# Kernel tuning notes

Hardware: AMD Instinct MI355X
Metric: run time of the kernel (lower is better)

Reference implementation:

```python
import jax, jax.numpy as jnp
import numpy as np

B, T, H = 2, 1024, 4096
HK, HV, DK, DV = 8, 32, 64, 64
VPK = HV // HK            # value heads per key head = 4
KEY_DIM = HK * DK         # 512
VAL_DIM = HV * DV         # 2048
CONV_DIM = 2 * KEY_DIM + VAL_DIM  # 3072
KSZ = 4
EPS = 1e-5
L2_EPS = 1e-6


def _l2norm(x):
    return x * jax.lax.rsqrt(jnp.sum(x * x, axis=-1, keepdims=True) + L2_EPS)


def setup_inputs() -> dict:
    key = jax.random.key(0)
    ks = jax.random.split(key, 8)
    s = 0.02
    return {
        "hidden_states": jax.random.normal(ks[0], (B, T, H), jnp.float32),
        "W_qkvz": jax.random.normal(ks[1], (H, 2 * KEY_DIM + 2 * VAL_DIM), jnp.float32) * s,
        "W_ba": jax.random.normal(ks[2], (H, 2 * HV), jnp.float32) * s,
        "conv_w": jax.random.normal(ks[3], (CONV_DIM, KSZ), jnp.float32) * 0.1,
        "dt_bias": jnp.ones((HV,), jnp.float32),
        "A_log": jnp.log(jax.random.uniform(ks[4], (HV,), jnp.float32, 1.0, 16.0)),
        "norm_w": jnp.ones((DV,), jnp.float32),
        "W_out": jax.random.normal(ks[5], (VAL_DIM, H), jnp.float32) * s,
    }


def _forward(hidden_states, W_qkvz, W_ba, conv_w, dt_bias, A_log, norm_w, W_out):
    # --- projections ---
    qkvz = hidden_states @ W_qkvz                       # [B,T,5120]
    ba = hidden_states @ W_ba                           # [B,T,64]
    # fix_query_key_value_ordering: per key head [q(Dk), k(Dk), v(vpk*Dv), z(vpk*Dv)]
    qkvz = qkvz.reshape(B, T, HK, 2 * DK + 2 * VPK * DV)
    q = qkvz[..., :DK]                                  # [B,T,HK,DK]
    k = qkvz[..., DK:2 * DK]
    v = qkvz[..., 2 * DK:2 * DK + VPK * DV].reshape(B, T, HV, DV)
    z = qkvz[..., 2 * DK + VPK * DV:].reshape(B, T, HV, DV)
    ba = ba.reshape(B, T, HK, 2 * VPK)
    b = ba[..., :VPK].reshape(B, T, HV)
    a = ba[..., VPK:].reshape(B, T, HV)

    # --- causal depthwise conv over concatenated qkv, then silu ---
    mixed = jnp.concatenate(
        [q.reshape(B, T, KEY_DIM), k.reshape(B, T, KEY_DIM), v.reshape(B, T, VAL_DIM)], axis=-1)
    padded = jnp.pad(mixed, ((0, 0), (KSZ - 1, 0), (0, 0)))
    conv = sum(padded[:, j:j + T, :] * conv_w[:, j] for j in range(KSZ))
    conv = jax.nn.silu(conv)
    q = conv[..., :KEY_DIM].reshape(B, T, HK, DK)
    k = conv[..., KEY_DIM:2 * KEY_DIM].reshape(B, T, HK, DK)
    v = conv[..., 2 * KEY_DIM:].reshape(B, T, HV, DV)

    # --- fused GDN gating: g = -exp(A_log)*softplus(a+dt_bias), beta = sigmoid(b) ---
    g = -jnp.exp(A_log) * jax.nn.softplus(a + dt_bias)  # [B,T,HV]
    beta = jax.nn.sigmoid(b)                            # [B,T,HV]

    # --- q/k l2 norm + scale, broadcast key heads to value heads ---
    q = _l2norm(q) * (DK ** -0.5)
    k = _l2norm(k)
    q = jnp.repeat(q, VPK, axis=2)                      # [B,T,HV,DK]
    k = jnp.repeat(k, VPK, axis=2)

    # --- gated delta-rule recurrence over time ---
    def step(S, inp):
        qt, kt, vt, gt, bt = inp                        # qt/kt [B,HV,DK], vt [B,HV,DV]
        S = S * jnp.exp(gt)[..., None, None]            # decay
        pred = jnp.einsum('bhk,bhkv->bhv', kt, S)
        delta = (vt - pred) * bt[..., None]
        S = S + jnp.einsum('bhk,bhv->bhkv', kt, delta)
        o = jnp.einsum('bhk,bhkv->bhv', qt, S)
        return S, o

    xs = (q.transpose(1, 0, 2, 3), k.transpose(1, 0, 2, 3), v.transpose(1, 0, 2, 3),
          g.transpose(1, 0, 2), beta.transpose(1, 0, 2))
    S0 = jnp.zeros((B, HV, DK, DV), q.dtype)
    _, o = jax.lax.scan(step, S0, xs)                   # [T,B,HV,DV]
    o = o.transpose(1, 0, 2, 3)                         # [B,T,HV,DV]

    # --- gated RMSNorm (norm before gate) + out projection ---
    o_n = o * jax.lax.rsqrt(jnp.mean(o * o, axis=-1, keepdims=True) + EPS) * norm_w
    o_n = o_n * jax.nn.silu(z)
    return o_n.reshape(B, T, VAL_DIM) @ W_out           # [B,T,H]


def reference(hidden_states, W_qkvz, W_ba, conv_w, dt_bias, A_log, norm_w, W_out):
    return _forward(hidden_states, W_qkvz, W_ba, conv_w, dt_bias, A_log, norm_w, W_out)
```

## Files before the change

kernel.cpp:

```cpp
#include <hip/hip_runtime.h>
#include <hip/hip_bf16.h>
#include <cstdint>
#include <cstddef>


typedef __attribute__((ext_vector_type(8))) short short8;
typedef __attribute__((ext_vector_type(4))) float f32x4;

__device__ __forceinline__ short f2bf(float f) {
  union { float f; unsigned u; } x; x.f = f;
  unsigned r = x.u + 0x7fffu + ((x.u >> 16) & 1u);
  return (short)(r >> 16);
}

__device__ __forceinline__ void gl_lds16(const short* g, short* l) {
  __builtin_amdgcn_global_load_lds(
      (const __attribute__((address_space(1))) void*)g,
      (__attribute__((address_space(3))) void*)l, 16, 0, 0);
}

__global__ __launch_bounds__(256) void to_bf16_kernel(const float* __restrict__ x,
                                                      short* __restrict__ y) {
  int i = blockIdx.x * 256 + threadIdx.x;
  float4 v = ((const float4*)x)[i];
  ushort4 r;
  r.x = (unsigned short)f2bf(v.x);
  r.y = (unsigned short)f2bf(v.y);
  r.z = (unsigned short)f2bf(v.z);
  r.w = (unsigned short)f2bf(v.w);
  ((ushort4*)y)[i] = r;
}

__global__ __launch_bounds__(256) void transpose_w1(const float* __restrict__ Wq,
                                                    const float* __restrict__ Wba,
                                                    short* __restrict__ Wt) {
  __shared__ float tile[32][33];
  int n0 = blockIdx.x * 32;
  int k0 = blockIdx.y * 32;
  int t = threadIdx.x;
  int r = t >> 5;
  int c = t & 31;
#pragma unroll
  for (int i = 0; i < 4; ++i) {
    int kl = r + i * 8;
    int n = n0 + c;
    float v = 0.f;
    if (n < 5120) v = Wq[(size_t)(k0 + kl) * 5120 + n];
    else if (n < 5184) v = Wba[(size_t)(k0 + kl) * 64 + (n - 5120)];
    tile[kl][c] = v;
  }
  __syncthreads();
#pragma unroll
  for (int i = 0; i < 4; ++i) {
    int nl = r + i * 8;
    int kl = c;
    Wt[(size_t)(n0 + nl) * 4096 + k0 + kl] = f2bf(tile[kl][nl]);
  }
}

__global__ __launch_bounds__(256) void transpose_w2(const float* __restrict__ W,
                                                    short* __restrict__ Wt) {
  __shared__ float tile[32][33];
  int n0 = blockIdx.x * 32;
  int k0 = blockIdx.y * 32;
  int t = threadIdx.x;
  int r = t >> 5;
  int c = t & 31;
#pragma unroll
  for (int i = 0; i < 4; ++i) {
    int kl = r + i * 8;
    tile[kl][c] = W[(size_t)(k0 + kl) * 4096 + n0 + c];
  }
  __syncthreads();
#pragma unroll
  for (int i = 0; i < 4; ++i) {
    int nl = r + i * 8;
    int kl = c;
    Wt[(size_t)(n0 + nl) * 2048 + k0 + kl] = f2bf(tile[kl][nl]);
  }
}

template <bool GUARD_N>
__global__ __launch_bounds__(512) void gemm256(const short* __restrict__ A,
                                               const short* __restrict__ Bt,
                                               float* __restrict__ C,
                                               int M, int N, int K) {
  __shared__ __align__(16) short As[3 * 8192];
  __shared__ __align__(16) short Bs[3 * 8192];
  const int tid = threadIdx.x;
  const int w = tid >> 6, lane = tid & 63;
  const int wm = w >> 2, wn = w & 3;
  const int m0 = blockIdx.x * 256, n0 = blockIdx.y * 256;
  (void)M;

  const int p0 = w * 64 + lane;
  const int rp0 = p0 >> 3, q0 = p0 & 7;
  const int mm0 = q0 ^ (rp0 & 7);
  const int srow = rp0 * 2 + (mm0 >> 2);
  const int scol = (mm0 & 3) << 3;
  const short* Ag = A + (size_t)(m0 + srow) * K + scol;
  const short* Bg = Bt + (size_t)(n0 + srow) * K + scol;
  const size_t rstep = (size_t)128 * K;

  const int fr = lane & 15;
  const int s = lane >> 4;
  int aoff[8], boff[4];
#pragma unroll
  for (int i = 0; i < 8; ++i) {
    int row = wm * 128 + i * 16 + fr;
    int rp = row >> 1;
    int q = (((row & 1) << 2) | s) ^ (rp & 7);
    aoff[i] = (rp * 8 + q) * 8;
  }
#pragma unroll
  for (int j = 0; j < 4; ++j) {
    int row = wn * 64 + j * 16 + fr;
    int rp = row >> 1;
    int q = (((row & 1) << 2) | s) ^ (rp & 7);
    boff[j] = (rp * 8 + q) * 8;
  }

  f32x4 acc[8][4];
#pragma unroll
  for (int i = 0; i < 8; ++i)
#pragma unroll
    for (int j = 0; j < 4; ++j) acc[i][j] = (f32x4){0.f, 0.f, 0.f, 0.f};

  const int NKT = K >> 5;

#define STAGE_A(kt, bb)                                                \
  { const short* g = Ag + (size_t)(kt) * 32;                           \
    gl_lds16(g,         &As[(bb) * 8192 + w * 512]);                   \
    gl_lds16(g + rstep, &As[(bb) * 8192 + 4096 + w * 512]); }
#define STAGE_B(kt, bb)                                                \
  { const short* g = Bg + (size_t)(kt) * 32;                           \
    gl_lds16(g,         &Bs[(bb) * 8192 + w * 512]);                   \
    gl_lds16(g + rstep, &Bs[(bb) * 8192 + 4096 + w * 512]); }

  STAGE_A(0, 0); STAGE_B(0, 0);
  STAGE_A(1, 1); STAGE_B(1, 1);
  asm volatile("s_waitcnt vmcnt(4)" ::: "memory");
  __builtin_amdgcn_s_barrier();
  __builtin_amdgcn_sched_barrier(0);

  int bi = 0;
  for (int kt = 0; kt < NKT; ++kt) {
    int bi2 = bi - 1; if (bi2 < 0) bi2 = 2;
    const short* Ab = &As[bi * 8192];
    const short* Bb = &Bs[bi * 8192];
    short8 af[4], bf[4];
#pragma unroll
    for (int i = 0; i < 4; ++i) af[i] = *(const short8*)&Ab[aoff[i]];
#pragma unroll
    for (int j = 0; j < 4; ++j) bf[j] = *(const short8*)&Bb[boff[j]];
    if (kt + 2 < NKT) STAGE_A(kt + 2, bi2);
    __builtin_amdgcn_s_barrier();
    asm volatile("s_waitcnt lgkmcnt(0)" ::: "memory");
    __builtin_amdgcn_sched_barrier(0);
    __builtin_amdgcn_s_setprio(1);
#pragma unroll
    for (int i = 0; i < 4; ++i)
#pragma unroll
      for (int j = 0; j < 4; ++j)
        acc[i][j] = __builtin_amdgcn_mfma_f32_16x16x32_bf16(af[i], bf[j], acc[i][j], 0, 0, 0);
    __builtin_amdgcn_s_setprio(0);
    __builtin_amdgcn_sched_barrier(0);
#pragma unroll
    for (int i = 0; i < 4; ++i) af[i] = *(const short8*)&Ab[aoff[i + 4]];
    if (kt + 2 < NKT) STAGE_B(kt + 2, bi2);
    if (kt < NKT - 2) { asm volatile("s_waitcnt vmcnt(4)" ::: "memory"); }
    else              { asm volatile("s_waitcnt vmcnt(0)" ::: "memory"); }
    __builtin_amdgcn_s_barrier();
    asm volatile("s_waitcnt lgkmcnt(0)" ::: "memory");
    __builtin_amdgcn_sched_barrier(0);
    __builtin_amdgcn_s_setprio(1);
#pragma unroll
    for (int i = 0; i < 4; ++i)
#pragma unroll
      for (int j = 0; j < 4; ++j)
        acc[i + 4][j] = __builtin_amdgcn_mfma_f32_16x16x32_bf16(af[i], bf[j], acc[i + 4][j], 0, 0, 0);
    __builtin_amdgcn_s_setprio(0);
    __builtin_amdgcn_sched_barrier(0);
    __builtin_amdgcn_s_barrier();
    ++bi; if (bi == 3) bi = 0;
  }
#undef STAGE_A
#undef STAGE_B

  const int rbase = (lane >> 4) << 2;
#pragma unroll
  for (int i = 0; i < 8; ++i) {
#pragma unroll
    for (int j = 0; j < 4; ++j) {
      int col = n0 + wn * 64 + j * 16 + fr;
      if (GUARD_N && col >= N) continue;
      int row = m0 + wm * 128 + i * 16 + rbase;
#pragma unroll
      for (int r = 0; r < 4; ++r)
        C[(size_t)(row + r) * N + col] = acc[i][j][r];
    }
  }
}

template <bool GUARD_N>
__global__ __launch_bounds__(256) void gemm128(const short* __restrict__ A,
                                               const short* __restrict__ Bt,
                                               float* __restrict__ C,
                                               int M, int N, int K) {
  __shared__ __align__(16) short As[128 * 32];
  __shared__ __align__(16) short Bs[128 * 32];
  const int tid = threadIdx.x;
  const int wave = tid >> 6;
  const int lane = tid & 63;
  const int m0 = blockIdx.x * 128;
  const int n0 = blockIdx.y * 128;
  const int wm = (wave >> 1) << 6;
  const int wn = (wave & 1) << 6;

  const int srow = (wave << 4) + (lane >> 2);
  const int scol = (lane & 3) << 3;
  const short* Ag = A + (size_t)(m0 + srow) * K + scol;
  const short* Bg = Bt + (size_t)(n0 + srow) * K + scol;
  const size_t rstep = (size_t)64 * K;

  const int fr = lane & 15;
  const int kq = (lane >> 4) << 3;

  f32x4 acc[4][4];
#pragma unroll
  for (int i = 0; i < 4; ++i)
#pragma unroll
    for (int j = 0; j < 4; ++j) acc[i][j] = (f32x4){0.f, 0.f, 0.f, 0.f};

  for (int k0 = 0; k0 < K; k0 += 32) {
    __syncthreads();
    gl_lds16(Ag + k0,         &As[wave * 512]);
    gl_lds16(Ag + rstep + k0, &As[2048 + wave * 512]);
    gl_lds16(Bg + k0,         &Bs[wave * 512]);
    gl_lds16(Bg + rstep + k0, &Bs[2048 + wave * 512]);
    __syncthreads();
    short8 af[4], bf[4];
#pragma unroll
    for (int i = 0; i < 4; ++i) {
      af[i] = *(const short8*)&As[(wm + i * 16 + fr) * 32 + kq];
      bf[i] = *(const short8*)&Bs[(wn + i * 16 + fr) * 32 + kq];
    }
#pragma unroll
    for (int mt = 0; mt < 4; ++mt)
#pragma unroll
      for (int nt = 0; nt < 4; ++nt)
        acc[mt][nt] = __builtin_amdgcn_mfma_f32_16x16x32_bf16(af[mt], bf[nt], acc[mt][nt], 0, 0, 0);
  }

  const int rbase = (lane >> 4) << 2;
#pragma unroll
  for (int mt = 0; mt < 4; ++mt) {
#pragma unroll
    for (int nt = 0; nt < 4; ++nt) {
      int ncol = n0 + wn + nt * 16 + fr;
      if (GUARD_N && ncol >= N) continue;
      int mrow = m0 + wm + mt * 16 + rbase;
#pragma unroll
      for (int r = 0; r < 4; ++r)
        C[(size_t)(mrow + r) * N + ncol] = acc[mt][nt][r];
    }
  }
}

__global__ __launch_bounds__(256) void conv_kernel(const float* __restrict__ qkvz,
                                                   const float* __restrict__ conv_w,
                                                   float* __restrict__ mix) {
  __shared__ float sq[1024];
  __shared__ float scale[16];
  int bt = blockIdx.x;
  int t = bt & 1023;
  int tid = threadIdx.x;
  for (int c = tid; c < 3072; c += 256) {
    int col;
    if (c < 512) {
      col = (c >> 6) * 640 + (c & 63);
    } else if (c < 1024) {
      int c2 = c - 512;
      col = (c2 >> 6) * 640 + 64 + (c2 & 63);
    } else {
      int c3 = c - 1024;
      int hv = c3 >> 6;
      col = (hv >> 2) * 640 + 128 + (hv & 3) * 64 + (c3 & 63);
    }
    float acc = 0.f;
#pragma unroll
    for (int j = 0; j < 4; ++j) {
      int tt = t - 3 + j;
      if (tt >= 0) acc += qkvz[(size_t)(bt - 3 + j) * 5184 + col] * conv_w[c * 4 + j];
    }
    float sv = acc / (1.f + __expf(-acc));
    if (c < 1024)
      sq[c] = sv;
    else
      mix[(size_t)bt * 3072 + c] = sv;
  }
  __syncthreads();
  int g = tid >> 4, l = tid & 15;
  float p = 0.f;
#pragma unroll
  for (int i = 0; i < 4; ++i) {
    float v = sq[g * 64 + l * 4 + i];
    p += v * v;
  }
  p += __shfl_xor(p, 1);
  p += __shfl_xor(p, 2);
  p += __shfl_xor(p, 4);
  p += __shfl_xor(p, 8);
  if (l == 0) scale[g] = rsqrtf(p + 1e-6f);
  __syncthreads();
  for (int c = tid; c < 1024; c += 256) {
    float s = scale[c >> 6] * ((c < 512) ? 0.125f : 1.f);
    mix[(size_t)bt * 3072 + c] = sq[c] * s;
  }
}

__global__ __launch_bounds__(256) void gate_kernel(const float* __restrict__ qkvz,
                                                   const float* __restrict__ dt_bias,
                                                   const float* __restrict__ A_log,
                                                   float* __restrict__ gb,
                                                   float* __restrict__ beta) {
  int i = blockIdx.x * 256 + threadIdx.x;
  int hv = i & 31;
  int bt = i >> 5;
  int hk = hv >> 2, vp = hv & 3;
  const float* row = qkvz + (size_t)bt * 5184 + 5120 + hk * 8;
  float bv = row[vp];
  float av = row[4 + vp];
  float x = av + dt_bias[hv];
  float sp = (x > 20.f) ? x : log1pf(expf(x));
  gb[i] = -expf(A_log[hv]) * sp;
  beta[i] = 1.f / (1.f + expf(-bv));
}

__global__ __launch_bounds__(256) void precompute_kernel(
    const float* __restrict__ mix, const float* __restrict__ gbuf,
    const float* __restrict__ betab, float* __restrict__ Wbuf,
    float* __restrict__ Pbuf, float* __restrict__ Rbuf, float* __restrict__ cbuf) {
  __shared__ float Kt[64][68];
  __shared__ float Vb[64][68];
  __shared__ float AM[64][68];
  __shared__ float Mm[64][68];
  __shared__ float Tb[16][17];
  __shared__ float cs[64], bb[64];

  const int u = blockIdx.x;
  const int chunk = u & 15, hv = (u >> 4) & 31, b = u >> 9;
  const int hk = hv >> 2;
  const int t0g = b * 1024 + chunk * 64;
  const int tid = threadIdx.x;
  const int tr = tid >> 2, q4 = tid & 3;

  {
    const float* mrow = mix + (size_t)(t0g + tr) * 3072;
#pragma unroll
    for (int e = 0; e < 4; ++e) {
      int c0 = q4 * 16 + e * 4;
      float4 kv = *(const float4*)(mrow + 512 + hk * 64 + c0);
      Kt[c0 + 0][tr] = kv.x; Kt[c0 + 1][tr] = kv.y;
      Kt[c0 + 2][tr] = kv.z; Kt[c0 + 3][tr] = kv.w;
      *(float4*)&Vb[tr][c0] = *(const float4*)(mrow + 1024 + hv * 64 + c0);
    }
  }
  if (tid < 64) {
    cs[tid] = gbuf[(size_t)(t0g + tid) * 32 + hv];
    bb[tid] = betab[(size_t)(t0g + tid) * 32 + hv];
  }
  __syncthreads();
  for (int off = 1; off < 64; off <<= 1) {
    float v = 0.f;
    if (tid < 64 && tid >= off) v = cs[tid - off];
    __syncthreads();
    if (tid < 64) cs[tid] += v;
    __syncthreads();
  }
  if (tid < 64) cbuf[(size_t)u * 64 + tid] = cs[tid];

  {
    float acc[16];
#pragma unroll
    for (int i = 0; i < 16; ++i) acc[i] = 0.f;
    for (int d = 0; d < 64; ++d) {
      float kv = Kt[d][tr];
#pragma unroll
      for (int e = 0; e < 4; ++e) {
        float4 ks = *(const float4*)&Kt[d][q4 * 16 + e * 4];
        acc[e * 4 + 0] += kv * ks.x; acc[e * 4 + 1] += kv * ks.y;
        acc[e * 4 + 2] += kv * ks.z; acc[e * 4 + 3] += kv * ks.w;
      }
    }
    float bt_ = bb[tr], ct_ = cs[tr];
#pragma unroll
    for (int j = 0; j < 16; ++j) {
      int s = q4 * 16 + j;
      AM[tr][s] = (s < tr) ? bt_ * acc[j] * __expf(ct_ - cs[s]) : 0.f;
    }
  }
  __syncthreads();

  for (int i = tid; i < 64 * 68; i += 256) (&Mm[0][0])[i] = 0.f;
  __syncthreads();
  if (tid < 64) {
    int blk = tid >> 4, j = tid & 15, base = blk * 16;
    Mm[base][base + j] = (j == 0) ? 1.f : 0.f;
    for (int r = 1; r < 16; ++r) {
      float sum = 0.f;
      for (int s = 0; s < r; ++s) sum += AM[base + r][base + s] * Mm[base + s][base + j];
      Mm[base + r][base + j] = ((r == j) ? 1.f : 0.f) - sum;
    }
  }
  __syncthreads();
  for (int d = 1; d < 4; ++d) {
    for (int j = 0; j + d < 4; ++j) {
      int i = j + d;
      int r = tid >> 4, c = tid & 15;
      float tsum = 0.f;
      for (int kb = j; kb < i; ++kb)
        for (int uu = 0; uu < 16; ++uu)
          tsum += AM[i * 16 + r][kb * 16 + uu] * Mm[kb * 16 + uu][j * 16 + c];
      Tb[r][c] = tsum;
      __syncthreads();
      float msum = 0.f;
      for (int uu = 0; uu < 16; ++uu)
        msum += Mm[i * 16 + r][i * 16 + uu] * Tb[uu][c];
      __syncthreads();
      Mm[i * 16 + r][j * 16 + c] = -msum;
      __syncthreads();
    }
  }

  {
    const float* mrow = mix + (size_t)(t0g + tr) * 3072 + hk * 64;
#pragma unroll
    for (int e = 0; e < 4; ++e) {
      int c0 = q4 * 16 + e * 4;
      float4 qv = *(const float4*)(mrow + c0);
      AM[c0 + 0][tr] = qv.x; AM[c0 + 1][tr] = qv.y;
      AM[c0 + 2][tr] = qv.z; AM[c0 + 3][tr] = qv.w;
    }
  }
  __syncthreads();

  {
    float acc[16];
#pragma unroll
    for (int i = 0; i < 16; ++i) acc[i] = 0.f;
    for (int d = 0; d < 64; ++d) {
      float qv = AM[d][tr];
#pragma unroll
      for (int e = 0; e < 4; ++e) {
        float4 ks = *(const float4*)&Kt[d][q4 * 16 + e * 4];
        acc[e * 4 + 0] += qv * ks.x; acc[e * 4 + 1] += qv * ks.y;
        acc[e * 4 + 2] += qv * ks.z; acc[e * 4 + 3] += qv * ks.w;
      }
    }
    float ct_ = cs[tr];
#pragma unroll
    for (int e = 0; e < 4; ++e) {
      int s0 = q4 * 16 + e * 4;
      float4 pv;
      pv.x = (s0 + 0 <= tr) ? acc[e * 4 + 0] * __expf(ct_ - cs[s0 + 0]) : 0.f;
      pv.y = (s0 + 1 <= tr) ? acc[e * 4 + 1] * __expf(ct_ - cs[s0 + 1]) : 0.f;
      pv.z = (s0 + 2 <= tr) ? acc[e * 4 + 2] * __expf(ct_ - cs[s0 + 2]) : 0.f;
      pv.w = (s0 + 3 <= tr) ? acc[e * 4 + 3] * __expf(ct_ - cs[s0 + 3]) : 0.f;
      *(float4*)&Pbuf[(size_t)u * 4096 + tr * 64 + s0] = pv;
    }
  }
  __syncthreads();

  {
    float vals[16];
#pragma unroll
    for (int j = 0; j < 16; ++j) vals[j] = Kt[q4 * 16 + j][tr];
    float sc = bb[tr] * __expf(cs[tr]);
    __syncthreads();
#pragma unroll
    for (int j = 0; j < 16; ++j) Kt[tr][q4 * 16 + j] = vals[j] * sc;
  }
  __syncthreads();

  {
    float acc[16];
#pragma unroll
    for (int i = 0; i < 16; ++i) acc[i] = 0.f;
    for (int s = 0; s < 64; ++s) {
      float m = Mm[tr][s];
#pragma unroll
      for (int e = 0; e < 4; ++e) {
        float4 kk = *(const float4*)&Kt[s][q4 * 16 + e * 4];
        acc[e * 4 + 0] += m * kk.x; acc[e * 4 + 1] += m * kk.y;
        acc[e * 4 + 2] += m * kk.z; acc[e * 4 + 3] += m * kk.w;
      }
    }
#pragma unroll
    for (int e = 0; e < 4; ++e) {
      float4 wv = {acc[e * 4 + 0], acc[e * 4 + 1], acc[e * 4 + 2], acc[e * 4 + 3]};
      *(float4*)&Wbuf[(size_t)u * 4096 + tr * 64 + q4 * 16 + e * 4] = wv;
    }
  }
  {
    float acc[16];
#pragma unroll
    for (int i = 0; i < 16; ++i) acc[i] = 0.f;
    for (int s = 0; s < 64; ++s) {
      float m = Mm[tr][s] * bb[s];
#pragma unroll
      for (int e = 0; e < 4; ++e) {
        float4 vv = *(const float4*)&Vb[s][q4 * 16 + e * 4];
        acc[e * 4 + 0] += m * vv.x; acc[e * 4 + 1] += m * vv.y;
        acc[e * 4 + 2] += m * vv.z; acc[e * 4 + 3] += m * vv.w;
      }
    }
#pragma unroll
    for (int e = 0; e < 4; ++e) {
      float4 rv = {acc[e * 4 + 0], acc[e * 4 + 1], acc[e * 4 + 2], acc[e * 4 + 3]};
      *(float4*)&Rbuf[(size_t)u * 4096 + tr * 64 + q4 * 16 + e * 4] = rv;
    }
  }
}

__global__ __launch_bounds__(512) void chunk_scan_kernel(
    const float* __restrict__ mix, const float* __restrict__ Wbuf,
    const float* __restrict__ Pbuf, const float* __restrict__ Rbuf,
    const float* __restrict__ cbuf, float* __restrict__ o) {
  __shared__ float Wb[64][68], Pb[64][68], Qh[64][68], Kt[64][68];
  __shared__ float St[16][68], Dt[16][68];
  __shared__ float cs[64];

  const int bid = blockIdx.x;
  const int vs = bid & 3, hv = (bid >> 2) & 31, b = bid >> 7;
  const int hk = hv >> 2;
  const int bh = b * 32 + hv;
  const int ubase = bh * 16;
  const int tid = threadIdx.x;
  const int tr = tid >> 3, q8 = tid & 7;
  const int c0 = q8 * 2, c1 = q8 * 2 + 1;

  for (int i = tid; i < 16 * 68; i += 512) (&St[0][0])[i] = 0.f;

  float4 WN[2], PN[2], KN[2], QN[2];
  float2 RN;
  float cN = 0.f;
  float e63c = 1.f;

#define ISSUE_LOADS(c)                                                          \
  {                                                                             \
    size_t uu = (size_t)(ubase + (c));                                          \
    _Pragma("unroll") for (int i = 0; i < 2; ++i) {                             \
      WN[i] = ((const float4*)(Wbuf + uu * 4096))[tid + 512 * i];               \
      PN[i] = ((const float4*)(Pbuf + uu * 4096))[tid + 512 * i];               \
    }                                                                           \
    const float* mrow = mix + (size_t)(b * 1024 + (c) * 64 + tr) * 3072;        \
    _Pragma("unroll") for (int e = 0; e < 2; ++e) {                             \
      KN[e] = *(const float4*)(mrow + 512 + hk * 64 + q8 * 8 + e * 4);          \
      QN[e] = *(const float4*)(mrow + hk * 64 + q8 * 8 + e * 4);                \
    }                                                                           \
    RN = *(const float2*)(Rbuf + uu * 4096 + tr * 64 + vs * 16 + q8 * 2);       \
    if (tid < 64) cN = cbuf[uu * 64 + tid];                                     \
  }

#define COMMIT()                                                                \
  {                                                                             \
    _Pragma("unroll") for (int i = 0; i < 2; ++i) {                             \
      int flat = (tid + 512 * i) * 4;                                           \
      int rr = flat >> 6, cc = flat & 63;                                       \
      *(float4*)&Wb[rr][cc] = WN[i];                                            \
      *(float4*)&Pb[rr][cc] = PN[i];                                            \
    }                                                                           \
    if (tid < 64) cs[tid] = cN;                                                 \
    __syncthreads();                                                            \
    float csv = cs[tr], cs63 = cs[63];                                          \
    float sQv = __expf(csv), sKv = __expf(cs63 - csv);                          \
    e63c = __expf(cs63);                                                        \
    float4 qa, qb;                                                              \
    qa.x = QN[0].x * sQv; qa.y = QN[0].y * sQv;                                 \
    qa.z = QN[0].z * sQv; qa.w = QN[0].w * sQv;                                 \
    qb.x = QN[1].x * sQv; qb.y = QN[1].y * sQv;                                 \
    qb.z = QN[1].z * sQv; qb.w = QN[1].w * sQv;                                 \
    *(float4*)&Qh[tr][q8 * 8] = qa;                                             \
    *(float4*)&Qh[tr][q8 * 8 + 4] = qb;                                         \
    Kt[q8 * 8 + 0][tr] = KN[0].x * sKv;                                         \
    Kt[q8 * 8 + 1][tr] = KN[0].y * sKv;                                         \
    Kt[q8 * 8 + 2][tr] = KN[0].z * sKv;                                         \
    Kt[q8 * 8 + 3][tr] = KN[0].w * sKv;                                         \
    Kt[q8 * 8 + 4][tr] = KN[1].x * sKv;                                         \
    Kt[q8 * 8 + 5][tr] = KN[1].y * sKv;                                         \
    Kt[q8 * 8 + 6][tr] = KN[1].z * sKv;                                         \
    Kt[q8 * 8 + 7][tr] = KN[1].w * sKv;                                         \
  }

  ISSUE_LOADS(0);
  COMMIT();
  float2 Rv = RN;

  for (int c = 0; c < 16; ++c) {
    if (c < 15) ISSUE_LOADS(c + 1);
    float2 acc = Rv;
#pragma unroll 4
    for (int k = 0; k < 64; k += 4) {
      float4 w4 = *(const float4*)&Wb[tr][k];
      float4 sa = *(const float4*)&St[c0][k];
      float4 sb = *(const float4*)&St[c1][k];
      acc.x -= w4.x * sa.x + w4.y * sa.y + w4.z * sa.z + w4.w * sa.w;
      acc.y -= w4.x * sb.x + w4.y * sb.y + w4.z * sb.z + w4.w * sb.w;
    }
    Dt[c0][tr] = acc.x;
    Dt[c1][tr] = acc.y;
    __syncthreads();
    {
      float2 ao = {0.f, 0.f};
#pragma unroll 4
      for (int i = 0; i < 64; i += 4) {
        float4 p4 = *(const float4*)&Pb[tr][i];
        float4 q4 = *(const float4*)&Qh[tr][i];
        float4 da = *(const float4*)&Dt[c0][i];
        float4 db = *(const float4*)&Dt[c1][i];
        float4 sa = *(const float4*)&St[c0][i];
        float4 sb = *(const float4*)&St[c1][i];
        ao.x += p4.x * da.x + p4.y * da.y + p4.z * da.z + p4.w * da.w
              + q4.x * sa.x + q4.y * sa.y + q4.z * sa.z + q4.w * sa.w;
        ao.y += p4.x * db.x + p4.y * db.y + p4.z * db.z + p4.w * db.w
              + q4.x * sb.x + q4.y * sb.y + q4.z * sb.z + q4.w * sb.w;
      }
      *(float2*)&o[((size_t)(bh * 4 + vs) * 1024 + c * 64 + tr) * 16 + q8 * 2] = ao;
    }
    __syncthreads();
    {
      float sx = St[c0][tr] * e63c;
      float sy = St[c1][tr] * e63c;
#pragma unroll 4
      for (int t = 0; t < 64; t += 4) {
        float4 k4 = *(const float4*)&Kt[tr][t];
        float4 da = *(const float4*)&Dt[c0][t];
        float4 db = *(const float4*)&Dt[c1][t];
        sx += k4.x * da.x + k4.y * da.y + k4.z * da.z + k4.w * da.w;
        sy += k4.x * db.x + k4.y * db.y + k4.z * db.z + k4.w * db.w;
      }
      St[c0][tr] = sx;
      St[c1][tr] = sy;
    }
    if (c < 15) {
      COMMIT();
      Rv = RN;
    }
  }
#undef ISSUE_LOADS
#undef COMMIT
}

__global__ __launch_bounds__(256) void rms_gate_kernel(const float* __restrict__ o,
                                                       const float* __restrict__ qkvz,
                                                       const float* __restrict__ norm_w,
                                                       short* __restrict__ on) {
  int bid = blockIdx.x;
  int bh = bid >> 8;
  int tg = bid & 255;
  int b = bh >> 5, hv = bh & 31;
  int t = tg * 4 + (threadIdx.x >> 6);
  int d = threadIdx.x & 63;
  int bt = b * 1024 + t;
  int hk = hv >> 2, vp = hv & 3;
  float x = o[((size_t)(bh * 4 + (d >> 4)) * 1024 + t) * 16 + (d & 15)];
  float ss = x * x;
  ss += __shfl_xor(ss, 1);
  ss += __shfl_xor(ss, 2);
  ss += __shfl_xor(ss, 4);
  ss += __shfl_xor(ss, 8);
  ss += __shfl_xor(ss, 16);
  ss += __shfl_xor(ss, 32);
  float sc = rsqrtf(ss * (1.f / 64.f) + 1e-5f);
  float z = qkvz[(size_t)bt * 5184 + hk * 640 + 384 + vp * 64 + d];
  float val = x * sc * norm_w[d] * (z / (1.f + __expf(-z)));
  on[((size_t)bt * 32 + hv) * 64 + d] = f2bf(val);
}

extern "C" void kernel_launch(void* const* d_in, const int* in_sizes, int n_in,
                              void* d_out, int out_size, void* d_ws, size_t ws_size,
                              hipStream_t stream) {
  const float* hidden = (const float*)d_in[0];
  const float* W_qkvz = (const float*)d_in[1];
  const float* W_ba = (const float*)d_in[2];
  const float* conv_w = (const float*)d_in[3];
  const float* dt_bias = (const float*)d_in[4];
  const float* A_log = (const float*)d_in[5];
  const float* norm_w = (const float*)d_in[6];
  const float* W_out = (const float*)d_in[7];
  float* out = (float*)d_out;

  char* ws = (char*)d_ws;
  short* A_bf = (short*)(ws + 0);
  short* Wt1 = (short*)(ws + 16777216);
  short* Wt2 = (short*)(ws + 59768832);
  float* qkvz = (float*)(ws + 76546048);
  float* mix = (float*)(ws + 119013376);
  float* gbuf = (float*)(ws + 144179200);
  float* beta = (float*)(ws + 144441344);
  float* o = (float*)(ws + 144703488);
  short* on = (short*)(ws + 161480704);
  float* Wbuf = (float*)(ws + 169869312);
  float* Pbuf = (float*)(ws + 186646528);
  float* Rbuf = (float*)(ws + 203423744);
  float* cbuf = (float*)(ws + 220200960);

  to_bf16_kernel<<<8192, 256, 0, stream>>>(hidden, A_bf);
  transpose_w1<<<dim3(164, 128), 256, 0, stream>>>(W_qkvz, W_ba, Wt1);
  transpose_w2<<<dim3(128, 64), 256, 0, stream>>>(W_out, Wt2);
  gemm256<true><<<dim3(8, 21), 512, 0, stream>>>(A_bf, Wt1, qkvz, 2048, 5184, 4096);
  conv_kernel<<<2048, 256, 0, stream>>>(qkvz, conv_w, mix);
  gate_kernel<<<256, 256, 0, stream>>>(qkvz, dt_bias, A_log, gbuf, beta);
  precompute_kernel<<<1024, 256, 0, stream>>>(mix, gbuf, beta, Wbuf, Pbuf, Rbuf, cbuf);
  chunk_scan_kernel<<<256, 512, 0, stream>>>(mix, Wbuf, Pbuf, Rbuf, cbuf, o);
  rms_gate_kernel<<<16384, 256, 0, stream>>>(o, qkvz, norm_w, on);
  gemm128<false><<<dim3(16, 32), 256, 0, stream>>>(on, Wt2, out, 2048, 4096, 2048);
}
```

Before: 599.7 us.

## Replace both GEMMs with pipelined 128x128 kernel using grid swizzle

Measured after the change: 562.6 us. 1.07x faster.

```diff
diff --git a/kernel.cpp b/kernel.cpp
--- a/kernel.cpp
+++ b/kernel.cpp
@@ -81,17 +81,21 @@
 }
 
 template <bool GUARD_N>
-__global__ __launch_bounds__(512) void gemm256(const short* __restrict__ A,
-                                               const short* __restrict__ Bt,
-                                               float* __restrict__ C,
-                                               int M, int N, int K) {
-  __shared__ __align__(16) short As[3 * 8192];
-  __shared__ __align__(16) short Bs[3 * 8192];
+__global__ __launch_bounds__(256) void gemm128p(const short* __restrict__ A,
+                                                const short* __restrict__ Bt,
+                                                float* __restrict__ C,
+                                                int N, int K, int MT) {
+  __shared__ __align__(16) short As[3 * 4096];
+  __shared__ __align__(16) short Bs[3 * 4096];
   const int tid = threadIdx.x;
   const int w = tid >> 6, lane = tid & 63;
-  const int wm = w >> 2, wn = w & 3;
-  const int m0 = blockIdx.x * 256, n0 = blockIdx.y * 256;
-  (void)M;
+  const int wm = w >> 1, wn = w & 1;
+
+  const int nwg = gridDim.x;
+  const int bid = blockIdx.x;
+  const int swz = (bid & 7) * (nwg >> 3) + (bid >> 3);
+  const int m0 = (swz % MT) * 128;
+  const int n0 = (swz / MT) * 128;
 
   const int p0 = w * 64 + lane;
   const int rp0 = p0 >> 3, q0 = p0 & 7;
@@ -100,14 +104,14 @@
   const int scol = (mm0 & 3) << 3;
   const short* Ag = A + (size_t)(m0 + srow) * K + scol;
   const short* Bg = Bt + (size_t)(n0 + srow) * K + scol;
-  const size_t rstep = (size_t)128 * K;
+  const size_t rstep = (size_t)64 * K;
 
   const int fr = lane & 15;
   const int s = lane >> 4;
-  int aoff[8], boff[4];
-#pragma unroll
-  for (int i = 0; i < 8; ++i) {
-    int row = wm * 128 + i * 16 + fr;
+  int aoff[4], boff[4];
+#pragma unroll
+  for (int i = 0; i < 4; ++i) {
+    int row = wm * 64 + i * 16 + fr;
     int rp = row >> 1;
     int q = (((row & 1) << 2) | s) ^ (rp & 7);
     aoff[i] = (rp * 8 + q) * 8;
@@ -120,9 +124,9 @@
     boff[j] = (rp * 8 + q) * 8;
   }
 
-  f32x4 acc[8][4];
-#pragma unroll
-  for (int i = 0; i < 8; ++i)
+  f32x4 acc[4][4];
+#pragma unroll
+  for (int i = 0; i < 4; ++i)
 #pragma unroll
     for (int j = 0; j < 4; ++j) acc[i][j] = (f32x4){0.f, 0.f, 0.f, 0.f};
 
@@ -130,12 +134,12 @@
 
 #define STAGE_A(kt, bb)                                                \
   { const short* g = Ag + (size_t)(kt) * 32;                           \
-    gl_lds16(g,         &As[(bb) * 8192 + w * 512]);                   \
-    gl_lds16(g + rstep, &As[(bb) * 8192 + 4096 + w * 512]); }
+    gl_lds16(g,         &As[(bb) * 4096 + w * 512]);                   \
+    gl_lds16(g + rstep, &As[(bb) * 4096 + 2048 + w * 512]); }
 #define STAGE_B(kt, bb)                                                \
   { const short* g = Bg + (size_t)(kt) * 32;                           \
-    gl_lds16(g,         &Bs[(bb) * 8192 + w * 512]);                   \
-    gl_lds16(g + rstep, &Bs[(bb) * 8192 + 4096 + w * 512]); }
+    gl_lds16(g,         &Bs[(bb) * 4096 + w * 512]);                   \
+    gl_lds16(g + rstep, &Bs[(bb) * 4096 + 2048 + w * 512]); }
 
   STAGE_A(0, 0); STAGE_B(0, 0);
   STAGE_A(1, 1); STAGE_B(1, 1);
@@ -146,11 +150,11 @@
   int bi = 0;
   for (int kt = 0; kt < NKT; ++kt) {
     int bi2 = bi - 1; if (bi2 < 0) bi2 = 2;
-    const short* Ab = &As[bi * 8192];
-    const short* Bb = &Bs[bi * 8192];
-    short8 af[4], bf[4];
-#pragma unroll
-    for (int i = 0; i < 4; ++i) af[i] = *(const short8*)&Ab[aoff[i]];
+    const short* Ab = &As[bi * 4096];
+    const short* Bb = &Bs[bi * 4096];
+    short8 af[2], bf[4];
+#pragma unroll
+    for (int i = 0; i < 2; ++i) af[i] = *(const short8*)&Ab[aoff[i]];
 #pragma unroll
     for (int j = 0; j < 4; ++j) bf[j] = *(const short8*)&Bb[boff[j]];
     if (kt + 2 < NKT) STAGE_A(kt + 2, bi2);
@@ -159,14 +163,14 @@
     __builtin_amdgcn_sched_barrier(0);
     __builtin_amdgcn_s_setprio(1);
 #pragma unroll
-    for (int i = 0; i < 4; ++i)
+    for (int i = 0; i < 2; ++i)
 #pragma unroll
       for (int j = 0; j < 4; ++j)
         acc[i][j] = __builtin_amdgcn_mfma_f32_16x16x32_bf16(af[i], bf[j], acc[i][j], 0, 0, 0);
     __builtin_amdgcn_s_setprio(0);
     __builtin_amdgcn_sched_barrier(0);
 #pragma unroll
-    for (int i = 0; i < 4; ++i) af[i] = *(const short8*)&Ab[aoff[i + 4]];
+    for (int i = 0; i < 2; ++i) af[i] = *(const short8*)&Ab[aoff[i + 2]];
     if (kt + 2 < NKT) STAGE_B(kt + 2, bi2);
     if (kt < NKT - 2) { asm volatile("s_waitcnt vmcnt(4)" ::: "memory"); }
     else              { asm volatile("s_waitcnt vmcnt(0)" ::: "memory"); }
@@ -175,10 +179,10 @@
     __builtin_amdgcn_sched_barrier(0);
     __builtin_amdgcn_s_setprio(1);
 #pragma unroll
-    for (int i = 0; i < 4; ++i)
+    for (int i = 0; i < 2; ++i)
 #pragma unroll
       for (int j = 0; j < 4; ++j)
-        acc[i + 4][j] = __builtin_amdgcn_mfma_f32_16x16x32_bf16(af[i], bf[j], acc[i + 4][j], 0, 0, 0);
+        acc[i + 2][j] = __builtin_amdgcn_mfma_f32_16x16x32_bf16(af[i], bf[j], acc[i + 2][j], 0, 0, 0);
     __builtin_amdgcn_s_setprio(0);
     __builtin_amdgcn_sched_barrier(0);
     __builtin_amdgcn_s_barrier();
@@ -189,80 +193,15 @@
 
   const int rbase = (lane >> 4) << 2;
 #pragma unroll
-  for (int i = 0; i < 8; ++i) {
+  for (int i = 0; i < 4; ++i) {
 #pragma unroll
     for (int j = 0; j < 4; ++j) {
       int col = n0 + wn * 64 + j * 16 + fr;
       if (GUARD_N && col >= N) continue;
-      int row = m0 + wm * 128 + i * 16 + rbase;
+      int row = m0 + wm * 64 + i * 16 + rbase;
 #pragma unroll
       for (int r = 0; r < 4; ++r)
         C[(size_t)(row + r) * N + col] = acc[i][j][r];
-    }
-  }
-}
-
-template <bool GUARD_N>
-__global__ __launch_bounds__(256) void gemm128(const short* __restrict__ A,
-                                               const short* __restrict__ Bt,
-                                               float* __restrict__ C,
-                                               int M, int N, int K) {
-  __shared__ __align__(16) short As[128 * 32];
-  __shared__ __align__(16) short Bs[128 * 32];
-  const int tid = threadIdx.x;
-  const int wave = tid >> 6;
-  const int lane = tid & 63;
-  const int m0 = blockIdx.x * 128;
-  const int n0 = blockIdx.y * 128;
-  const int wm = (wave >> 1) << 6;
-  const int wn = (wave & 1) << 6;
-
-  const int srow = (wave << 4) + (lane >> 2);
-  const int scol = (lane & 3) << 3;
-  const short* Ag = A + (size_t)(m0 + srow) * K + scol;
-  const short* Bg = Bt + (size_t)(n0 + srow) * K + scol;
-  const size_t rstep = (size_t)64 * K;
-
-  const int fr = lane & 15;
-  const int kq = (lane >> 4) << 3;
-
-  f32x4 acc[4][4];
-#pragma unroll
-  for (int i = 0; i < 4; ++i)
-#pragma unroll
-    for (int j = 0; j < 4; ++j) acc[i][j] = (f32x4){0.f, 0.f, 0.f, 0.f};
-
-  for (int k0 = 0; k0 < K; k0 += 32) {
-    __syncthreads();
-    gl_lds16(Ag + k0,         &As[wave * 512]);
-    gl_lds16(Ag + rstep + k0, &As[2048 + wave * 512]);
-    gl_lds16(Bg + k0,         &Bs[wave * 512]);
-    gl_lds16(Bg + rstep + k0, &Bs[2048 + wave * 512]);
-    __syncthreads();
-    short8 af[4], bf[4];
-#pragma unroll
-    for (int i = 0; i < 4; ++i) {
-      af[i] = *(const short8*)&As[(wm + i * 16 + fr) * 32 + kq];
-      bf[i] = *(const short8*)&Bs[(wn + i * 16 + fr) * 32 + kq];
-    }
-#pragma unroll
-    for (int mt = 0; mt < 4; ++mt)
-#pragma unroll
-      for (int nt = 0; nt < 4; ++nt)
-        acc[mt][nt] = __builtin_amdgcn_mfma_f32_16x16x32_bf16(af[mt], bf[nt], acc[mt][nt], 0, 0, 0);
-  }
-
-  const int rbase = (lane >> 4) << 2;
-#pragma unroll
-  for (int mt = 0; mt < 4; ++mt) {
-#pragma unroll
-    for (int nt = 0; nt < 4; ++nt) {
-      int ncol = n0 + wn + nt * 16 + fr;
-      if (GUARD_N && ncol >= N) continue;
-      int mrow = m0 + wm + mt * 16 + rbase;
-#pragma unroll
-      for (int r = 0; r < 4; ++r)
-        C[(size_t)(mrow + r) * N + ncol] = acc[mt][nt][r];
     }
   }
 }
@@ -709,11 +648,11 @@
   to_bf16_kernel<<<8192, 256, 0, stream>>>(hidden, A_bf);
   transpose_w1<<<dim3(164, 128), 256, 0, stream>>>(W_qkvz, W_ba, Wt1);
   transpose_w2<<<dim3(128, 64), 256, 0, stream>>>(W_out, Wt2);
-  gemm256<true><<<dim3(8, 21), 512, 0, stream>>>(A_bf, Wt1, qkvz, 2048, 5184, 4096);
+  gemm128p<true><<<656, 256, 0, stream>>>(A_bf, Wt1, qkvz, 5184, 4096, 16);
   conv_kernel<<<2048, 256, 0, stream>>>(qkvz, conv_w, mix);
   gate_kernel<<<256, 256, 0, stream>>>(qkvz, dt_bias, A_log, gbuf, beta);
   precompute_kernel<<<1024, 256, 0, stream>>>(mix, gbuf, beta, Wbuf, Pbuf, Rbuf, cbuf);
   chunk_scan_kernel<<<256, 512, 0, stream>>>(mix, Wbuf, Pbuf, Rbuf, cbuf, o);
   rms_gate_kernel<<<16384, 256, 0, stream>>>(o, qkvz, norm_w, on);
-  gemm128<false><<<dim3(16, 32), 256, 0, stream>>>(on, Wt2, out, 2048, 4096, 2048);
-}
+  gemm128p<false><<<512, 256, 0, stream>>>(on, Wt2, out, 4096, 2048, 16);
+}
```
